# Performance work log

Hardware: AMD Instinct MI355X
Metric: run time of the kernel (lower is better)

## Reference

```python
import jax, jax.numpy as jnp
import numpy as np

B, S, D, K, R = 64, 512, 768, 8, 277
D_K = 64  # attention scale dim from original module (self.d_k)


def setup_inputs() -> dict:
    key = jax.random.key(0)
    ks = jax.random.split(key, 10)
    sc = 1.0 / np.sqrt(D)
    return {
        "embedding": jax.random.normal(ks[0], (B, S, D), dtype=jnp.float32),
        "h_span": jnp.sort(jax.random.randint(ks[1], (B, 2), 0, S), axis=-1).astype(jnp.int32),
        "t_span": jnp.sort(jax.random.randint(ks[2], (B, 2), 0, S), axis=-1).astype(jnp.int32),
        "b_spans": jnp.sort(jax.random.randint(ks[3], (B, K, 2), 0, S), axis=-1).astype(jnp.int32),
        "wu_w": jax.random.normal(ks[4], (D, D), dtype=jnp.float32) * sc,
        "wu_b": jnp.zeros((D,), jnp.float32),
        "wv_w": jax.random.normal(ks[5], (D, D), dtype=jnp.float32) * sc,
        "wv_b": jnp.zeros((D,), jnp.float32),
        "wi_w": jax.random.normal(ks[6], (D, D), dtype=jnp.float32) * sc,
        "wi_b": jnp.zeros((D,), jnp.float32),
        "ln1_w": jax.random.normal(ks[7], (D, D), dtype=jnp.float32) * sc,
        "ln1_b": jnp.zeros((D,), jnp.float32),
        "pred_w": jax.random.normal(ks[8], (R, D), dtype=jnp.float32) * sc,
        "pred_b": jnp.zeros((R,), jnp.float32),
    }


def _span_max(emb, span):
    # emb: [B, S, D]; span: [B, 2] inclusive [start, end] (start <= end).
    pos = jnp.arange(emb.shape[1])[None, :]          # [1, S]
    m = (pos >= span[:, :1]) & (pos <= span[:, 1:])  # [B, S]
    return jnp.max(jnp.where(m[:, :, None], emb, -jnp.inf), axis=1)  # [B, D]


def reference(embedding, h_span, t_span, b_spans,
              wu_w, wu_b, wv_w, wv_b, wi_w, wi_b,
              ln1_w, ln1_b, pred_w, pred_b):
    # Ragged entity-span max-pooling (torch.max over embedding[dp, s:e+1]).
    h_emb = _span_max(embedding, h_span)   # [B, D]
    t_emb = _span_max(embedding, t_span)   # [B, D]
    # K is a small fixed structural count (bridge subsampling cap); loop is fine.
    b_emb = jnp.stack([_span_max(embedding, b_spans[:, k, :]) for k in range(K)], axis=1)  # [B, K, D]

    # wu/wv/wi attention-style multi-hop path aggregation.
    u = h_emb @ wu_w.T + wu_b              # [B, D]
    v = t_emb @ wv_w.T + wv_b              # [B, D]
    bi = jnp.einsum('bkd,ed->bke', b_emb, wi_w) + wi_b  # [B, K, D]
    att = jax.nn.softmax(jnp.einsum('bd,bkd->bk', u, bi) / np.sqrt(D_K), axis=-1)  # [B, K]
    ctx = jnp.einsum('bk,bkd->bd', att, bi)  # [B, D]

    pair = jax.nn.relu((u + v + ctx) @ ln1_w.T + ln1_b)  # [B, D]
    logits = pair @ pred_w.T + pred_b                    # [B, R]
    return logits
```

## Files before the change

kernel.cpp:

```cpp
#include <hip/hip_runtime.h>
#include <hip/hip_bf16.h>

#define B 64
#define S 512
#define D 768
#define K 8
#define R 277
#define NSPAN 10
#define M_TOT 640
#define DD (D*D)

typedef unsigned short ushort_t;
typedef __attribute__((ext_vector_type(8))) short short8;
typedef __attribute__((ext_vector_type(4))) float f32x4;

__device__ __forceinline__ ushort_t f2bf(float f) {
    unsigned u = __float_as_uint(f);
    unsigned r = (u + 0x7FFFu + ((u >> 16) & 1u)) >> 16;
    return (ushort_t)r;
}

template<int RPC, int NCH, int CVTY>
__global__ void k_pool1(const float* __restrict__ emb,
                        const float* __restrict__ wu,
                        const float* __restrict__ wv,
                        const float* __restrict__ wi,
                        const float* __restrict__ ln1_w,
                        const float* __restrict__ pred_w,
                        float* __restrict__ chunkmax,
                        ushort_t* __restrict__ wbf) {
    int b = blockIdx.x, c = blockIdx.y;
    int t = threadIdx.x;

    if (c >= NCH) {
        int g = (b * CVTY + (c - NCH)) * 192 + t;
        size_t e0 = (size_t)g * 8;
        const size_t TOT = (size_t)4*DD + (size_t)R*D;
        if (e0 < TOT) {
            const float* src; size_t off;
            if      (e0 < (size_t)DD)   { src = wu;     off = e0; }
            else if (e0 < (size_t)2*DD) { src = wv;     off = e0 - DD; }
            else if (e0 < (size_t)3*DD) { src = wi;     off = e0 - (size_t)2*DD; }
            else if (e0 < (size_t)4*DD) { src = ln1_w;  off = e0 - (size_t)3*DD; }
            else                        { src = pred_w; off = e0 - (size_t)4*DD; }
            float4 f0 = *(const float4*)(src + off);
            float4 f1 = *(const float4*)(src + off + 4);
            short8 o;
            o[0] = (short)f2bf(f0.x); o[1] = (short)f2bf(f0.y);
            o[2] = (short)f2bf(f0.z); o[3] = (short)f2bf(f0.w);
            o[4] = (short)f2bf(f1.x); o[5] = (short)f2bf(f1.y);
            o[6] = (short)f2bf(f1.z); o[7] = (short)f2bf(f1.w);
            *(short8*)&wbf[e0] = o;
        }
        return;
    }

    const float4* e4 = (const float4*)(emb + (size_t)b * S * D)
                     + (size_t)(c * RPC) * (D/4) + t;
    float4 m = make_float4(-INFINITY, -INFINITY, -INFINITY, -INFINITY);
    #pragma unroll
    for (int i = 0; i < RPC; ++i) {
        float4 v = e4[i * (D/4)];
        m.x = fmaxf(m.x, v.x); m.y = fmaxf(m.y, v.y);
        m.z = fmaxf(m.z, v.z); m.w = fmaxf(m.w, v.w);
    }
    *(float4*)(chunkmax + ((size_t)b * NCH + c) * D + t*4) = m;
}

template<int RPC, int NCH>
__global__ void k_pool2(const float* __restrict__ chunkmax,
                        const float* __restrict__ emb,
                        const int* __restrict__ h_span,
                        const int* __restrict__ t_span,
                        const int* __restrict__ b_spans,
                        ushort_t* __restrict__ pooled_bf) {
    int task = blockIdx.x;
    int b = task / NSPAN, j = task % NSPAN;
    int s0, s1, row;
    if (j == 0)      { s0 = h_span[b*2]; s1 = h_span[b*2+1]; row = b; }
    else if (j == 1) { s0 = t_span[b*2]; s1 = t_span[b*2+1]; row = B + b; }
    else {
        int k = j - 2;
        s0 = b_spans[(b*K+k)*2]; s1 = b_spans[(b*K+k)*2 + 1];
        row = 2*B + b*K + k;
    }
    int t = threadIdx.x;

    int c_lo = (s0 + RPC - 1) / RPC;
    int c_hi = (s1 + 1) / RPC - 1;

    float4 m = make_float4(-INFINITY, -INFINITY, -INFINITY, -INFINITY);
    const float4* cm = (const float4*)(chunkmax + (size_t)b * NCH * D) + t;
    for (int c = c_lo; c <= c_hi; ++c) {
        float4 v = cm[(size_t)c * (D/4)];
        m.x = fmaxf(m.x, v.x); m.y = fmaxf(m.y, v.y);
        m.z = fmaxf(m.z, v.z); m.w = fmaxf(m.w, v.w);
    }
    const float4* e4 = (const float4*)(emb + (size_t)b * S * D) + t;
    int h_end = min(s1, c_lo * RPC - 1);
    for (int s = s0; s <= h_end; ++s) {
        float4 v = e4[(size_t)s * (D/4)];
        m.x = fmaxf(m.x, v.x); m.y = fmaxf(m.y, v.y);
        m.z = fmaxf(m.z, v.z); m.w = fmaxf(m.w, v.w);
    }
    int t_beg = max(s0, (c_hi + 1) * RPC);
    for (int s = t_beg; s <= s1; ++s) {
        float4 v = e4[(size_t)s * (D/4)];
        m.x = fmaxf(m.x, v.x); m.y = fmaxf(m.y, v.y);
        m.z = fmaxf(m.z, v.z); m.w = fmaxf(m.w, v.w);
    }

    unsigned lo = (unsigned)f2bf(m.x) | ((unsigned)f2bf(m.y) << 16);
    unsigned hi = (unsigned)f2bf(m.z) | ((unsigned)f2bf(m.w) << 16);
    *(uint2*)&pooled_bf[(size_t)row * D + t*4] = make_uint2(lo, hi);
}

template<int KSPLIT>
__global__ __launch_bounds__(256)
void k_gemm_bf(const ushort_t* __restrict__ abf,
               const ushort_t* __restrict__ wbf,
               float* __restrict__ p_part) {
    __shared__ ushort_t Al[64][64];
    __shared__ ushort_t Bl[64][64];
    int e0 = blockIdx.x * 64;
    int m0 = blockIdx.y * 64;
    int dbase = blockIdx.z * (D / KSPLIT);
    const ushort_t* Wm = wbf + (size_t)((m0 < B) ? 0 : (m0 < 2*B) ? 1 : 2) * DD;

    int tid = threadIdx.x;
    int w = tid >> 6, l = tid & 63;
    int srow = tid >> 2;
    int sc   = tid & 3;

    const ushort_t* ga = abf + (size_t)(m0 + srow) * D + dbase;
    const ushort_t* gb = Wm  + (size_t)(e0 + srow) * D + dbase;
    int p0 = ((sc     ) ^ (srow & 7)) * 8;
    int p1 = ((sc + 4 ) ^ (srow & 7)) * 8;

    f32x4 acc[4] = {};
    const int NIT = (D / KSPLIT) / 64;
    short8 pa0 = *(const short8*)(ga + sc*8);
    short8 pa1 = *(const short8*)(ga + sc*8 + 32);
    short8 pb0 = *(const short8*)(gb + sc*8);
    short8 pb1 = *(const short8*)(gb + sc*8 + 32);

    for (int it = 0; it < NIT; ++it) {
        __syncthreads();
        *(short8*)&Al[srow][p0] = pa0;
        *(short8*)&Al[srow][p1] = pa1;
        *(short8*)&Bl[srow][p0] = pb0;
        *(short8*)&Bl[srow][p1] = pb1;
        __syncthreads();
        if (it + 1 < NIT) {
            ga += 64; gb += 64;
            pa0 = *(const short8*)(ga + sc*8);
            pa1 = *(const short8*)(ga + sc*8 + 32);
            pb0 = *(const short8*)(gb + sc*8);
            pb1 = *(const short8*)(gb + sc*8 + 32);
        }
        int g = l >> 4, x = l & 7;
        #pragma unroll
        for (int ks = 0; ks < 2; ++ks) {
            int chunk = ks*4 + g;
            short8 a = *(const short8*)&Al[w*16 + (l & 15)][(chunk ^ x) * 8];
            #pragma unroll
            for (int nt = 0; nt < 4; ++nt) {
                short8 bf = *(const short8*)&Bl[nt*16 + (l & 15)][(chunk ^ x) * 8];
                acc[nt] = __builtin_amdgcn_mfma_f32_16x16x32_bf16(a, bf, acc[nt], 0, 0, 0);
            }
        }
    }

    int r4 = (l >> 4) * 4, cc = l & 15;
    #pragma unroll
    for (int nt = 0; nt < 4; ++nt)
        #pragma unroll
        for (int r = 0; r < 4; ++r)
            p_part[((size_t)blockIdx.z * M_TOT + m0 + w*16 + r4 + r) * D + e0 + nt*16 + cc] = acc[nt][r];
}

template<int KSPLIT>
__global__ __launch_bounds__(512)
void k_att2(const float* __restrict__ p_part,
            const float* __restrict__ wu_b,
            const float* __restrict__ wv_b,
            const float* __restrict__ wi_b,
            const float* __restrict__ pred_b,
            ushort_t* __restrict__ s_bf,
            float* __restrict__ out) {
    __shared__ float U[D], V[D], BI[K][D];
    __shared__ float dots[K];
    int b = blockIdx.x, tid = threadIdx.x;

    for (int r = tid; r < R; r += 512) out[(size_t)b * R + r] = pred_b[r];

    for (int task = tid; task < NSPAN * (D/4); task += 512) {
        int j = task / (D/4), sl = task % (D/4);
        size_t row = (j == 0) ? (size_t)b : (j == 1) ? (size_t)(B + b)
                   : (size_t)(2*B + b*K + (j - 2));
        const float* bias = (j == 0) ? wu_b : (j == 1) ? wv_b : wi_b;
        float4 acc = *(const float4*)(bias + sl*4);
        #pragma unroll
        for (int ks = 0; ks < KSPLIT; ++ks) {
            float4 p = *(const float4*)(p_part + ((size_t)ks * M_TOT + row) * D + sl*4);
            acc.x += p.x; acc.y += p.y; acc.z += p.z; acc.w += p.w;
        }
        float* dst = (j == 0) ? U : (j == 1) ? V : BI[j-2];
        *(float4*)(dst + sl*4) = acc;
    }
    __syncthreads();

    int wave = tid >> 6, lane = tid & 63;
    {
        float part = 0.f;
        #pragma unroll
        for (int i = 0; i < D/64; ++i) {
            int d = i*64 + lane;
            part += U[d] * BI[wave][d];
        }
        #pragma unroll
        for (int off = 32; off > 0; off >>= 1) part += __shfl_xor(part, off);
        if (lane == 0) dots[wave] = part * 0.125f;
    }
    __syncthreads();

    float mx = -INFINITY;
    #pragma unroll
    for (int k = 0; k < K; ++k) mx = fmaxf(mx, dots[k]);
    float ex[K], sum = 0.f;
    #pragma unroll
    for (int k = 0; k < K; ++k) { ex[k] = expf(dots[k] - mx); sum += ex[k]; }
    float inv = 1.f / sum;
    for (int d = tid; d < D; d += 512) {
        float c = 0.f;
        #pragma unroll
        for (int k = 0; k < K; ++k) c += ex[k] * BI[k][d];
        s_bf[(size_t)b * D + d] = f2bf(U[d] + V[d] + c * inv);
    }
}

template<int KSPL>
__global__ __launch_bounds__(256)
void k_pairg_bf(const ushort_t* __restrict__ s_bf,
                const ushort_t* __restrict__ ln1_bf,
                float* __restrict__ pair_part) {
    __shared__ ushort_t Al[64][64];
    __shared__ ushort_t Bl[64][64];
    int e0 = blockIdx.x * 64;
    int dbase = blockIdx.y * (D / KSPL);

    int tid = threadIdx.x;
    int w = tid >> 6, l = tid & 63;
    int srow = tid >> 2;
    int sc   = tid & 3;

    const ushort_t* ga = s_bf   + (size_t)srow * D + dbase;
    const ushort_t* gb = ln1_bf + (size_t)(e0 + srow) * D + dbase;
    int p0 = ((sc     ) ^ (srow & 7)) * 8;
    int p1 = ((sc + 4 ) ^ (srow & 7)) * 8;

    f32x4 acc[4] = {};
    const int NIT = (D / KSPL) / 64;
    short8 pa0 = *(const short8*)(ga + sc*8);
    short8 pa1 = *(const short8*)(ga + sc*8 + 32);
    short8 pb0 = *(const short8*)(gb + sc*8);
    short8 pb1 = *(const short8*)(gb + sc*8 + 32);

    for (int it = 0; it < NIT; ++it) {
        __syncthreads();
        *(short8*)&Al[srow][p0] = pa0;
        *(short8*)&Al[srow][p1] = pa1;
        *(short8*)&Bl[srow][p0] = pb0;
        *(short8*)&Bl[srow][p1] = pb1;
        __syncthreads();
        if (it + 1 < NIT) {
            ga += 64; gb += 64;
            pa0 = *(const short8*)(ga + sc*8);
            pa1 = *(const short8*)(ga + sc*8 + 32);
            pb0 = *(const short8*)(gb + sc*8);
            pb1 = *(const short8*)(gb + sc*8 + 32);
        }
        int g = l >> 4, x = l & 7;
        #pragma unroll
        for (int ks = 0; ks < 2; ++ks) {
            int chunk = ks*4 + g;
            short8 a = *(const short8*)&Al[w*16 + (l & 15)][(chunk ^ x) * 8];
            #pragma unroll
            for (int nt = 0; nt < 4; ++nt) {
                short8 bf = *(const short8*)&Bl[nt*16 + (l & 15)][(chunk ^ x) * 8];
                acc[nt] = __builtin_amdgcn_mfma_f32_16x16x32_bf16(a, bf, acc[nt], 0, 0, 0);
            }
        }
    }

    int r4 = (l >> 4) * 4, cc = l & 15;
    #pragma unroll
    for (int nt = 0; nt < 4; ++nt)
        #pragma unroll
        for (int r = 0; r < 4; ++r)
            pair_part[((size_t)blockIdx.y * B + w*16 + r4 + r) * D + e0 + nt*16 + cc] = acc[nt][r];
}

template<int KSPP, int KSPL>
__global__ __launch_bounds__(256)
void k_predg_bf(const float* __restrict__ pair_part,
                const float* __restrict__ ln1_b,
                const ushort_t* __restrict__ pred_bf,
                float* __restrict__ out) {
    __shared__ ushort_t Al[64][64];
    __shared__ ushort_t Bl[64][64];
    int r0 = blockIdx.x * 64;
    int dbase = blockIdx.y * (D / KSPP);

    int tid = threadIdx.x;
    int w = tid >> 6, l = tid & 63;
    int srow = tid >> 2;
    int sc   = tid & 3;
    int p0 = ((sc     ) ^ (srow & 7)) * 8;
    int p1 = ((sc + 4 ) ^ (srow & 7)) * 8;

    auto build8 = [&](int off) -> short8 {
        float4 a0 = *(const float4*)(ln1_b + dbase + off);
        float4 a1 = *(const float4*)(ln1_b + dbase + off + 4);
        #pragma unroll
        for (int ks = 0; ks < KSPL; ++ks) {
            const float* p = pair_part + ((size_t)ks * B + srow) * D + dbase + off;
            float4 q0 = *(const float4*)p;
            float4 q1 = *(const float4*)(p + 4);
            a0.x += q0.x; a0.y += q0.y; a0.z += q0.z; a0.w += q0.w;
            a1.x += q1.x; a1.y += q1.y; a1.z += q1.z; a1.w += q1.w;
        }
        short8 o;
        o[0] = (short)f2bf(fmaxf(a0.x, 0.f)); o[1] = (short)f2bf(fmaxf(a0.y, 0.f));
        o[2] = (short)f2bf(fmaxf(a0.z, 0.f)); o[3] = (short)f2bf(fmaxf(a0.w, 0.f));
        o[4] = (short)f2bf(fmaxf(a1.x, 0.f)); o[5] = (short)f2bf(fmaxf(a1.y, 0.f));
        o[6] = (short)f2bf(fmaxf(a1.z, 0.f)); o[7] = (short)f2bf(fmaxf(a1.w, 0.f));
        return o;
    };

    short8 a0 = build8(sc*8);
    short8 a1 = build8(sc*8 + 32);
    int rw = r0 + srow; if (rw >= R) rw = R - 1;
    const ushort_t* gb = pred_bf + (size_t)rw * D + dbase;
    short8 pb0 = *(const short8*)(gb + sc*8);
    short8 pb1 = *(const short8*)(gb + sc*8 + 32);

    *(short8*)&Al[srow][p0] = a0;
    *(short8*)&Al[srow][p1] = a1;
    *(short8*)&Bl[srow][p0] = pb0;
    *(short8*)&Bl[srow][p1] = pb1;
    __syncthreads();

    f32x4 acc[4] = {};
    int g = l >> 4, x = l & 7;
    #pragma unroll
    for (int ks = 0; ks < 2; ++ks) {
        int chunk = ks*4 + g;
        short8 a = *(const short8*)&Al[w*16 + (l & 15)][(chunk ^ x) * 8];
        #pragma unroll
        for (int nt = 0; nt < 4; ++nt) {
            short8 bf = *(const short8*)&Bl[nt*16 + (l & 15)][(chunk ^ x) * 8];
            acc[nt] = __builtin_amdgcn_mfma_f32_16x16x32_bf16(a, bf, acc[nt], 0, 0, 0);
        }
    }

    int r4 = (l >> 4) * 4, cc = l & 15;
    #pragma unroll
    for (int nt = 0; nt < 4; ++nt) {
        int rr = r0 + nt*16 + cc;
        if (rr < R) {
            #pragma unroll
            for (int r = 0; r < 4; ++r)
                atomicAdd(&out[(size_t)(w*16 + r4 + r) * R + rr], acc[nt][r]);
        }
    }
}

extern "C" void kernel_launch(void* const* d_in, const int* in_sizes, int n_in,
                              void* d_out, int out_size, void* d_ws, size_t ws_size,
                              hipStream_t stream) {
    const float* emb     = (const float*)d_in[0];
    const int*   h_span  = (const int*)  d_in[1];
    const int*   t_span  = (const int*)  d_in[2];
    const int*   b_spans = (const int*)  d_in[3];
    const float* wu_w    = (const float*)d_in[4];
    const float* wu_b    = (const float*)d_in[5];
    const float* wv_w    = (const float*)d_in[6];
    const float* wv_b    = (const float*)d_in[7];
    const float* wi_w    = (const float*)d_in[8];
    const float* wi_b    = (const float*)d_in[9];
    const float* ln1_w   = (const float*)d_in[10];
    const float* ln1_b   = (const float*)d_in[11];
    const float* pred_w  = (const float*)d_in[12];
    const float* pred_b  = (const float*)d_in[13];
    float* out = (float*)d_out;

    const int KSPLIT = 2;
    const int KSPL   = 6;
    const int KSPP   = 12;
    const int NCH    = 64;
    const int RPC    = S / NCH;
    const int CVTY   = 27;

    float* ws = (float*)d_ws;
    ushort_t* pooled_bf = (ushort_t*)ws;
    ushort_t* wbf = (ushort_t*)(ws + (size_t)M_TOT*D/2);
    size_t wbf_fl = ((size_t)4*DD + (size_t)R*D + 1) / 2;
    float* p_part    = ws + (size_t)M_TOT*D/2 + wbf_fl;
    ushort_t* s_bf   = (ushort_t*)(p_part + (size_t)KSPLIT*M_TOT*D);
    float* pair_part = (float*)(s_bf + (size_t)B*D);
    float* chunkmax  = pair_part + (size_t)KSPL*B*D;
    (void)ws_size; (void)in_sizes; (void)n_in; (void)out_size;

    k_pool1<RPC, NCH, CVTY><<<dim3(B, NCH + CVTY), 192, 0, stream>>>(
        emb, wu_w, wv_w, wi_w, ln1_w, pred_w, chunkmax, wbf);
    k_pool2<RPC, NCH><<<M_TOT, 192, 0, stream>>>(
        chunkmax, emb, h_span, t_span, b_spans, pooled_bf);
    k_gemm_bf<KSPLIT><<<dim3(D/64, M_TOT/64, KSPLIT), 256, 0, stream>>>(pooled_bf, wbf, p_part);
    k_att2<KSPLIT><<<B, 512, 0, stream>>>(p_part, wu_b, wv_b, wi_b, pred_b, s_bf, out);
    k_pairg_bf<KSPL><<<dim3(D/64, KSPL), 256, 0, stream>>>(s_bf, wbf + (size_t)3*DD, pair_part);
    k_predg_bf<KSPP, KSPL><<<dim3((R+63)/64, KSPP), 256, 0, stream>>>(
        pair_part, ln1_b, wbf + (size_t)4*DD, out);
}
```

Before: 63.83 us.

## Replace two-pass chunked span max-pool with single direct span-scan kernel

Drops the chunk-max precompute pass that read all of the embedding, and instead has one block per span scan only the span's rows directly, 16 rows at a time with clamped indices. The weight bf16 conversion is folded into the same single launch as extra blocks. This removes a full embedding read and one kernel launch. In exchange, overlapping spans now reread the same rows, and long spans become serial per-block scans, which can cause load imbalance.

```diff
diff --git a/kernel.cpp b/kernel.cpp
--- a/kernel.cpp
+++ b/kernel.cpp
@@ -20,20 +20,21 @@
     return (ushort_t)r;
 }
 
-template<int RPC, int NCH, int CVTY>
-__global__ void k_pool1(const float* __restrict__ emb,
-                        const float* __restrict__ wu,
-                        const float* __restrict__ wv,
-                        const float* __restrict__ wi,
-                        const float* __restrict__ ln1_w,
-                        const float* __restrict__ pred_w,
-                        float* __restrict__ chunkmax,
-                        ushort_t* __restrict__ wbf) {
-    int b = blockIdx.x, c = blockIdx.y;
-    int t = threadIdx.x;
-
-    if (c >= NCH) {
-        int g = (b * CVTY + (c - NCH)) * 192 + t;
+__global__ void k_pool(const float* __restrict__ emb,
+                       const int* __restrict__ h_span,
+                       const int* __restrict__ t_span,
+                       const int* __restrict__ b_spans,
+                       const float* __restrict__ wu,
+                       const float* __restrict__ wv,
+                       const float* __restrict__ wi,
+                       const float* __restrict__ ln1_w,
+                       const float* __restrict__ pred_w,
+                       ushort_t* __restrict__ pooled_bf,
+                       ushort_t* __restrict__ wbf) {
+    int bid = blockIdx.x, t = threadIdx.x;
+
+    if (bid >= B * NSPAN) {
+        int g = (bid - B * NSPAN) * 192 + t;
         size_t e0 = (size_t)g * 8;
         const size_t TOT = (size_t)4*DD + (size_t)R*D;
         if (e0 < TOT) {
@@ -55,27 +56,7 @@
         return;
     }
 
-    const float4* e4 = (const float4*)(emb + (size_t)b * S * D)
-                     + (size_t)(c * RPC) * (D/4) + t;
-    float4 m = make_float4(-INFINITY, -INFINITY, -INFINITY, -INFINITY);
-    #pragma unroll
-    for (int i = 0; i < RPC; ++i) {
-        float4 v = e4[i * (D/4)];
-        m.x = fmaxf(m.x, v.x); m.y = fmaxf(m.y, v.y);
-        m.z = fmaxf(m.z, v.z); m.w = fmaxf(m.w, v.w);
-    }
-    *(float4*)(chunkmax + ((size_t)b * NCH + c) * D + t*4) = m;
-}
-
-template<int RPC, int NCH>
-__global__ void k_pool2(const float* __restrict__ chunkmax,
-                        const float* __restrict__ emb,
-                        const int* __restrict__ h_span,
-                        const int* __restrict__ t_span,
-                        const int* __restrict__ b_spans,
-                        ushort_t* __restrict__ pooled_bf) {
-    int task = blockIdx.x;
-    int b = task / NSPAN, j = task % NSPAN;
+    int b = bid / NSPAN, j = bid % NSPAN;
     int s0, s1, row;
     if (j == 0)      { s0 = h_span[b*2]; s1 = h_span[b*2+1]; row = b; }
     else if (j == 1) { s0 = t_span[b*2]; s1 = t_span[b*2+1]; row = B + b; }
@@ -84,30 +65,22 @@
         s0 = b_spans[(b*K+k)*2]; s1 = b_spans[(b*K+k)*2 + 1];
         row = 2*B + b*K + k;
     }
-    int t = threadIdx.x;
-
-    int c_lo = (s0 + RPC - 1) / RPC;
-    int c_hi = (s1 + 1) / RPC - 1;
+    int len = s1 - s0 + 1;
+    const float4* base = (const float4*)(emb + (size_t)b * S * D)
+                       + (size_t)s0 * (D/4) + t;
 
     float4 m = make_float4(-INFINITY, -INFINITY, -INFINITY, -INFINITY);
-    const float4* cm = (const float4*)(chunkmax + (size_t)b * NCH * D) + t;
-    for (int c = c_lo; c <= c_hi; ++c) {
-        float4 v = cm[(size_t)c * (D/4)];
-        m.x = fmaxf(m.x, v.x); m.y = fmaxf(m.y, v.y);
-        m.z = fmaxf(m.z, v.z); m.w = fmaxf(m.w, v.w);
-    }
-    const float4* e4 = (const float4*)(emb + (size_t)b * S * D) + t;
-    int h_end = min(s1, c_lo * RPC - 1);
-    for (int s = s0; s <= h_end; ++s) {
-        float4 v = e4[(size_t)s * (D/4)];
-        m.x = fmaxf(m.x, v.x); m.y = fmaxf(m.y, v.y);
-        m.z = fmaxf(m.z, v.z); m.w = fmaxf(m.w, v.w);
-    }
-    int t_beg = max(s0, (c_hi + 1) * RPC);
-    for (int s = t_beg; s <= s1; ++s) {
-        float4 v = e4[(size_t)s * (D/4)];
-        m.x = fmaxf(m.x, v.x); m.y = fmaxf(m.y, v.y);
-        m.z = fmaxf(m.z, v.z); m.w = fmaxf(m.w, v.w);
+    int niters = (len + 15) >> 4;
+    for (int it = 0; it < niters; ++it) {
+        int r0 = it * 16;
+        #pragma unroll
+        for (int i = 0; i < 16; ++i) {
+            int s = r0 + i;
+            s = (s < len) ? s : (len - 1);
+            float4 v = base[(size_t)s * (D/4)];
+            m.x = fmaxf(m.x, v.x); m.y = fmaxf(m.y, v.y);
+            m.z = fmaxf(m.z, v.z); m.w = fmaxf(m.w, v.w);
+        }
     }
 
     unsigned lo = (unsigned)f2bf(m.x) | ((unsigned)f2bf(m.y) << 16);
@@ -398,9 +371,7 @@
     const int KSPLIT = 2;
     const int KSPL   = 6;
     const int KSPP   = 12;
-    const int NCH    = 64;
-    const int RPC    = S / NCH;
-    const int CVTY   = 27;
+    const int CVTBLKS = (int)(((size_t)4*DD + (size_t)R*D) / 8 + 191) / 192;
 
     float* ws = (float*)d_ws;
     ushort_t* pooled_bf = (ushort_t*)ws;
@@ -409,13 +380,11 @@
     float* p_part    = ws + (size_t)M_TOT*D/2 + wbf_fl;
     ushort_t* s_bf   = (ushort_t*)(p_part + (size_t)KSPLIT*M_TOT*D);
     float* pair_part = (float*)(s_bf + (size_t)B*D);
-    float* chunkmax  = pair_part + (size_t)KSPL*B*D;
     (void)ws_size; (void)in_sizes; (void)n_in; (void)out_size;
 
-    k_pool1<RPC, NCH, CVTY><<<dim3(B, NCH + CVTY), 192, 0, stream>>>(
-        emb, wu_w, wv_w, wi_w, ln1_w, pred_w, chunkmax, wbf);
-    k_pool2<RPC, NCH><<<M_TOT, 192, 0, stream>>>(
-        chunkmax, emb, h_span, t_span, b_spans, pooled_bf);
+    k_pool<<<B*NSPAN + CVTBLKS, 192, 0, stream>>>(
+        emb, h_span, t_span, b_spans, wu_w, wv_w, wi_w, ln1_w, pred_w,
+        pooled_bf, wbf);
     k_gemm_bf<KSPLIT><<<dim3(D/64, M_TOT/64, KSPLIT), 256, 0, stream>>>(pooled_bf, wbf, p_part);
     k_att2<KSPLIT><<<B, 512, 0, stream>>>(p_part, wu_b, wv_b, wi_b, pred_b, s_bf, out);
     k_pairg_bf<KSPL><<<dim3(D/64, KSPL), 256, 0, stream>>>(s_bf, wbf + (size_t)3*DD, pair_part);
```

Measured after the change: 78.60 us. +23.1%, slower.
